# Kernel optimization log

Hardware: AMD Instinct MI355X
Metric: run time of the kernel (lower is better)

## Reference

```python
import jax, jax.numpy as jnp
import numpy as np

B, N, D, DH, H, L = 32768, 6, 128, 64, 4, 4  # batch, items, dim_inp, head/ffn dim, heads, encoders
SEQ = 4  # tokens kept by embeddings[:, :4, :]
EPS = 1e-5


def _layernorm(x, g, b):
    mu = jnp.mean(x, axis=-1, keepdims=True)
    var = jnp.mean((x - mu) ** 2, axis=-1, keepdims=True)
    return (x - mu) / jnp.sqrt(var + EPS) * g + b


def setup_inputs() -> dict:
    key = jax.random.key(0)
    ks = jax.random.split(key, 18)
    s = 0.05
    f32 = jnp.float32
    return {
        "embeddings": jax.random.normal(ks[0], (B, N, D), f32),
        # per-layer, per-head QKV projections: [L, H, D, DH]
        "wq": jax.random.normal(ks[1], (L, H, D, DH), f32) * s,
        "bq": jax.random.normal(ks[2], (L, H, DH), f32) * s,
        "wk": jax.random.normal(ks[3], (L, H, D, DH), f32) * s,
        "bk": jax.random.normal(ks[4], (L, H, DH), f32) * s,
        "wv": jax.random.normal(ks[5], (L, H, D, DH), f32) * s,
        "bv": jax.random.normal(ks[6], (L, H, DH), f32) * s,
        # output projection after head concat: [L, H*DH, D]
        "wo": jax.random.normal(ks[7], (L, H * DH, D), f32) * s,
        "bo": jax.random.normal(ks[8], (L, D), f32) * s,
        "ln1_g": jnp.ones((L, D), f32),
        "ln1_b": jnp.zeros((L, D), f32),
        # FFN: Linear(D, DH) -> GELU -> Linear(DH, D)
        "ff_w1": jax.random.normal(ks[9], (L, D, DH), f32) * s,
        "ff_b1": jax.random.normal(ks[10], (L, DH), f32) * s,
        "ff_w2": jax.random.normal(ks[11], (L, DH, D), f32) * s,
        "ff_b2": jax.random.normal(ks[12], (L, D), f32) * s,
        "ln2_g": jnp.ones((L, D), f32),
        "ln2_b": jnp.zeros((L, D), f32),
    }


def reference(embeddings, wq, bq, wk, bk, wv, bv, wo, bo,
              ln1_g, ln1_b, ff_w1, ff_b1, ff_w2, ff_b2, ln2_g, ln2_b):
    x = embeddings[:, :SEQ, :]          # [B, 4, D]
    positive_pair = embeddings[:, 4, :]  # [B, D]
    negative_pairs = embeddings[:, 5:, :]  # [B, 1, D]

    # Original AttentionHead scales by sqrt(seq_len) (query.size(1)), not sqrt(head_dim)
    scale = jnp.sqrt(jnp.asarray(SEQ, x.dtype))

    for l in range(L):
        # all heads batched into one einsum (same math as per-head Linear+bmm loop)
        q = jnp.einsum('bsd,hdf->bhsf', x, wq[l]) + bq[l][:, None, :]
        k = jnp.einsum('bsd,hdf->bhsf', x, wk[l]) + bk[l][:, None, :]
        v = jnp.einsum('bsd,hdf->bhsf', x, wv[l]) + bv[l][:, None, :]
        scores = jnp.einsum('bhsf,bhtf->bhst', q, k) / scale  # [B,H,4,4]
        attn = jax.nn.softmax(scores, axis=-1)
        ctx = jnp.einsum('bhst,bhtf->bhsf', attn, v)
        # torch.cat over heads along last dim == [B,S,H,DH] -> [B,S,H*DH]
        ctx = ctx.transpose(0, 2, 1, 3).reshape(x.shape[0], SEQ, H * DH)
        proj = ctx @ wo[l] + bo[l]
        context = _layernorm(x + proj, ln1_g[l], ln1_b[l])
        # FFN (dropout = identity in eval); GELU is exact (erf) as in torch default
        h = jax.nn.gelu(context @ ff_w1[l] + ff_b1[l], approximate=False)
        res = h @ ff_w2[l] + ff_b2[l]
        # NOTE: residual uses the PRE-attention input (faithful to Encoder.forward)
        x = _layernorm(res + x, ln2_g[l], ln2_b[l])

    final_embedding = x.mean(axis=-2)  # [B, D]
    return (final_embedding, positive_pair, negative_pairs)
```

## Files before the change

### kernel.cpp

```cpp
#include <hip/hip_runtime.h>
#include <stdint.h>


typedef __attribute__((ext_vector_type(8))) short    bf16x8;
typedef __attribute__((ext_vector_type(4))) _Float16 f16x4;
typedef __attribute__((ext_vector_type(4))) float    f32x4;

#define MFMA_BF(a,b,c) __builtin_amdgcn_mfma_f32_16x16x32_bf16((a),(b),(c),0,0,0)
#define MFMA_H(a,b,c)  __builtin_amdgcn_mfma_f32_16x16x16f16((a),(b),(c),0,0,0)

__device__ __forceinline__ unsigned short f2bf(float f){
  unsigned u = __float_as_uint(f);
  u += 0x7FFFu + ((u>>16)&1u);
  return (unsigned short)(u>>16);
}
__device__ __forceinline__ unsigned pk2bf(float a, float b){
  return (unsigned)f2bf(a) | ((unsigned)f2bf(b)<<16);
}
__device__ __forceinline__ unsigned pkh(float a, float b){
  auto h = __builtin_amdgcn_cvt_pkrtz(a, b);
  return __builtin_bit_cast(unsigned, h);
}
__device__ __forceinline__ void ubf2(unsigned u, float& a, float& b){
  a = __uint_as_float(u<<16);
  b = __uint_as_float(u & 0xffff0000u);
}

__global__ __launch_bounds__(256) void prep_kernel(
    const float* __restrict__ wq, const float* __restrict__ wk,
    const float* __restrict__ wv, const float* __restrict__ wo,
    const float* __restrict__ w1, const float* __restrict__ w2,
    unsigned short* __restrict__ ws){
  int e16 = blockIdx.x*256 + threadIdx.x;
  int t    = e16 >> 10;
  int c    = (e16 >> 6) & 15;
  int lane = e16 & 63;
  int lnid = lane & 15, qid = lane >> 4;
  int l = t/18, r = t - l*18;
  float v[8];
  if (r < 16){
    int h = r >> 2, ty = r & 3;
    if (ty < 3){
      const float* W = (ty==0? wq : (ty==1? wk : wv)) + (size_t)(l*4+h)*8192;
      int f = (c>>2)*16 + lnid, d0 = (c&3)*32 + qid*8;
      #pragma unroll
      for (int j=0;j<8;++j) v[j] = W[(d0+j)*64 + f];
    } else {
      const float* W = wo + (size_t)l*32768 + (size_t)h*8192;
      int dd = (c>>1)*16 + lnid, k0 = (c&1)*32 + qid*8;
      #pragma unroll
      for (int j=0;j<8;++j) v[j] = W[(k0+j)*128 + dd];
    }
  } else if (r == 16){
    const float* W = w1 + (size_t)l*8192;
    int f = (c>>2)*16 + lnid, d0 = (c&3)*32 + qid*8;
    #pragma unroll
    for (int j=0;j<8;++j) v[j] = W[(d0+j)*64 + f];
  } else {
    const float* W = w2 + (size_t)l*8192;
    int dd = (c>>1)*16 + lnid, k0 = (c&1)*32 + qid*8;
    #pragma unroll
    for (int j=0;j<8;++j) v[j] = W[(k0+j)*128 + dd];
  }
  uint4 o;
  o.x = pk2bf(v[0],v[1]); o.y = pk2bf(v[2],v[3]);
  o.z = pk2bf(v[4],v[5]); o.w = pk2bf(v[6],v[7]);
  ((uint4*)ws)[e16] = o;
}

#define XOFF  0
#define QOFF  4352
#define KOFF  6656
#define VOFF  8960
#define PG    11520
#define WSOFF 46080
#define SLOTSZ 16384
#define LDSSZ 78848

__global__ __launch_bounds__(256,2) void bert_kernel(
    const float* __restrict__ emb,
    const float* __restrict__ bq, const float* __restrict__ bk, const float* __restrict__ bv,
    const float* __restrict__ bo,
    const float* __restrict__ ln1g, const float* __restrict__ ln1b,
    const float* __restrict__ fb1, const float* __restrict__ fb2,
    const float* __restrict__ ln2g, const float* __restrict__ ln2b,
    const unsigned short* __restrict__ ws,
    float* __restrict__ out)
{
  __shared__ __align__(16) char smem[LDSSZ];
  const int tid  = threadIdx.x;
  const int wid  = tid>>6;
  const int lane = tid&63;
  const int lnid = lane&15;
  const int qid  = lane>>4;
  const int batch0 = blockIdx.x*16;
  char* gb = smem + wid*PG;
  const f32x4 ZV = {0.f,0.f,0.f,0.f};

  {
    int row = lane>>2, colq = (lane&3)*32;
    const float* src = emb + ((size_t)(batch0 + wid*4 + (row>>2))*6 + (row&3))*128 + colq;
    #pragma unroll
    for (int i=0;i<8;++i){
      float4 v = *(const float4*)(src + i*4);
      uint2 u; u.x = pk2bf(v.x,v.y); u.y = pk2bf(v.z,v.w);
      *(uint2*)(gb + XOFF + row*272 + (colq+i*4)*2) = u;
    }
  }
  {
    const float* eb = emb + (size_t)batch0*768;
    float* o1 = out + 4194304 + (size_t)batch0*128;
    float* o2 = out + 8388608 + (size_t)batch0*128;
    #pragma unroll
    for (int i=0;i<4;++i){
      int idx = i*256 + tid;
      int b = idx>>6, rem = idx&63;
      float4 v = *(const float4*)(eb + b*768 + 512 + rem*4);
      if (rem<32) *(float4*)(o1 + b*128 + rem*4) = v;
      else        *(float4*)(o2 + b*128 + (rem-32)*4) = v;
    }
  }

  const uint4* wsv = (const uint4*)ws;
  {
    #pragma unroll
    for (int i=0;i<4;++i)
      *(uint4*)(smem + WSOFF + (i*256+tid)*16) = wsv[i*256+tid];
  }
  __syncthreads();

  f32x4  pacc[8];
  bf16x8 xfrag[4];
  int sidx = 0;

  for (int l=0; l<4; ++l){
    #pragma unroll
    for (int kc=0;kc<4;++kc)
      xfrag[kc] = *(const bf16x8*)(gb + XOFF + lnid*272 + kc*64 + qid*16);
    #pragma unroll
    for (int nt=0;nt<8;++nt) pacc[nt] = ZV;

    for (int ph=0; ph<18; ++ph){
      char* slot = smem + WSOFF + (sidx&1)*SLOTSZ;

      uint4 pf0,pf1,pf2,pf3;
      bool havepf = (sidx+1 < 72);
      if (havepf){
        const uint4* p = wsv + (size_t)(sidx+1)*1024 + tid;
        pf0 = p[0]; pf1 = p[256]; pf2 = p[512]; pf3 = p[768];
      }

      if (ph < 16){
        int h = ph>>2, t = ph&3;
        if (t < 2){
          char* dst = gb + (t? KOFF : QOFF);
          const float* bias_base = (t? bk : bq) + (l*4+h)*64;
          #pragma unroll
          for (int nt=0; nt<4; ++nt){
            f32x4 a = ZV;
            #pragma unroll
            for (int kc=0; kc<4; ++kc){
              bf16x8 wf = *(const bf16x8*)(slot + (nt*4+kc)*1024 + lane*16);
              a = MFMA_BF(wf, xfrag[kc], a);
            }
            f32x4 bs = *(const f32x4*)(bias_base + nt*16 + qid*4);
            uint2 u; u.x = pk2bf(a[0]+bs[0], a[1]+bs[1]);
                     u.y = pk2bf(a[2]+bs[2], a[3]+bs[3]);
            *(uint2*)(dst + lnid*144 + nt*32 + qid*8) = u;
          }
        } else if (t == 2){
          const float* bias_base = bv + (l*4+h)*64;
          #pragma unroll
          for (int nt=0; nt<4; ++nt){
            f32x4 a = ZV;
            #pragma unroll
            for (int kc=0; kc<4; ++kc){
              bf16x8 wf = *(const bf16x8*)(slot + (nt*4+kc)*1024 + lane*16);
              a = MFMA_BF(xfrag[kc], wf, a);
            }
            float b = bias_base[nt*16 + lnid];
            uint2 u; u.x = pkh(a[0]+b, a[1]+b);
                     u.y = pkh(a[2]+b, a[3]+b);
            *(uint2*)(gb + VOFF + (nt*16+lnid)*40 + qid*8) = u;
          }
        } else {
          bf16x8 kf0 = *(const bf16x8*)(gb+KOFF + lnid*144 + qid*16);
          bf16x8 kf1 = *(const bf16x8*)(gb+KOFF + lnid*144 + 64 + qid*16);
          bf16x8 qf0 = *(const bf16x8*)(gb+QOFF + lnid*144 + qid*16);
          bf16x8 qf1 = *(const bf16x8*)(gb+QOFF + lnid*144 + 64 + qid*16);
          f32x4 st = MFMA_BF(kf0, qf0, ZV);
          st = MFMA_BF(kf1, qf1, st);
          float s0=st[0]*0.5f, s1=st[1]*0.5f, s2=st[2]*0.5f, s3=st[3]*0.5f;
          float mx = fmaxf(fmaxf(s0,s1), fmaxf(s2,s3));
          float p0=__expf(s0-mx), p1=__expf(s1-mx), p2=__expf(s2-mx), p3=__expf(s3-mx);
          float inv = 1.f/(p0+p1+p2+p3);
          bool valid = (lnid>>2) == qid;
          p0 = valid? p0*inv:0.f; p1 = valid? p1*inv:0.f;
          p2 = valid? p2*inv:0.f; p3 = valid? p3*inv:0.f;
          union { unsigned u[2]; f16x4 h4; } pu;
          pu.u[0] = pkh(p0,p1);
          pu.u[1] = pkh(p2,p3);
          f16x4 pf = pu.h4;
          #pragma unroll
          for (int ft=0; ft<4; ++ft){
            f16x4 vf = *(const f16x4*)(gb+VOFF + (ft*16+lnid)*40 + qid*8);
            f32x4 c = MFMA_H(vf, pf, ZV);
            uint2 u; u.x = pk2bf(c[0],c[1]); u.y = pk2bf(c[2],c[3]);
            *(uint2*)(gb+QOFF + lnid*144 + ft*32 + qid*8) = u;
          }
          asm volatile("" ::: "memory");
          bf16x8 c0 = *(const bf16x8*)(gb+QOFF + lnid*144 + qid*16);
          bf16x8 c1 = *(const bf16x8*)(gb+QOFF + lnid*144 + 64 + qid*16);
          #pragma unroll
          for (int nt=0; nt<8; ++nt){
            bf16x8 w0 = *(const bf16x8*)(slot + (nt*2+0)*1024 + lane*16);
            bf16x8 w1f= *(const bf16x8*)(slot + (nt*2+1)*1024 + lane*16);
            f32x4 a = pacc[nt];
            a = MFMA_BF(w0, c0, a);
            a = MFMA_BF(w1f, c1, a);
            pacc[nt] = a;
          }
        }
      } else if (ph == 16){
        float sm=0.f, sq=0.f;
        #pragma unroll
        for (int nt=0;nt<8;++nt){
          f32x4 b4 = *(const f32x4*)(bo + l*128 + nt*16 + qid*4);
          uint2 xr = *(const uint2*)(gb+XOFF + lnid*272 + nt*32 + qid*8);
          float x0,x1,x2,x3; ubf2(xr.x,x0,x1); ubf2(xr.y,x2,x3);
          f32x4 a = pacc[nt];
          a[0]+=b4[0]+x0; a[1]+=b4[1]+x1; a[2]+=b4[2]+x2; a[3]+=b4[3]+x3;
          sm += a[0]+a[1]+a[2]+a[3];
          sq += a[0]*a[0]+a[1]*a[1]+a[2]*a[2]+a[3]*a[3];
          pacc[nt] = a;
        }
        sm += __shfl_xor(sm,16); sq += __shfl_xor(sq,16);
        sm += __shfl_xor(sm,32); sq += __shfl_xor(sq,32);
        float mu = sm*(1.f/128.f);
        float rs = rsqrtf(sq*(1.f/128.f) - mu*mu + 1e-5f);
        #pragma unroll
        for (int nt=0;nt<8;++nt){
          f32x4 g4 = *(const f32x4*)(ln1g + l*128 + nt*16 + qid*4);
          f32x4 be = *(const f32x4*)(ln1b + l*128 + nt*16 + qid*4);
          f32x4 a = pacc[nt];
          float v0 = (a[0]-mu)*rs*g4[0]+be[0];
          float v1 = (a[1]-mu)*rs*g4[1]+be[1];
          float v2 = (a[2]-mu)*rs*g4[2]+be[2];
          float v3 = (a[3]-mu)*rs*g4[3]+be[3];
          uint2 u; u.x = pk2bf(v0,v1); u.y = pk2bf(v2,v3);
          *(uint2*)(gb+QOFF + lnid*272 + nt*32 + qid*8) = u;
        }
        asm volatile("" ::: "memory");
        bf16x8 x2f[4];
        #pragma unroll
        for (int kc=0;kc<4;++kc)
          x2f[kc] = *(const bf16x8*)(gb+QOFF + lnid*272 + kc*64 + qid*16);
        #pragma unroll
        for (int nt=0; nt<4; ++nt){
          f32x4 a = ZV;
          #pragma unroll
          for (int kc=0; kc<4; ++kc){
            bf16x8 wf = *(const bf16x8*)(slot + (nt*4+kc)*1024 + lane*16);
            a = MFMA_BF(wf, x2f[kc], a);
          }
          f32x4 b1 = *(const f32x4*)(fb1 + l*64 + nt*16 + qid*4);
          float g0,g1,g2,g3;
          { float x = a[0]+b1[0]; g0 = 0.5f*x*(1.f+erff(x*0.70710678f)); }
          { float x = a[1]+b1[1]; g1 = 0.5f*x*(1.f+erff(x*0.70710678f)); }
          { float x = a[2]+b1[2]; g2 = 0.5f*x*(1.f+erff(x*0.70710678f)); }
          { float x = a[3]+b1[3]; g3 = 0.5f*x*(1.f+erff(x*0.70710678f)); }
          uint2 u; u.x = pk2bf(g0,g1); u.y = pk2bf(g2,g3);
          *(uint2*)(gb+VOFF + lnid*144 + nt*32 + qid*8) = u;
        }
      } else {
        bf16x8 h0  = *(const bf16x8*)(gb+VOFF + lnid*144 + qid*16);
        bf16x8 h1f = *(const bf16x8*)(gb+VOFF + lnid*144 + 64 + qid*16);
        f32x4 racc[8];
        #pragma unroll
        for (int nt=0; nt<8; ++nt){
          bf16x8 w0 = *(const bf16x8*)(slot + (nt*2+0)*1024 + lane*16);
          bf16x8 w1f= *(const bf16x8*)(slot + (nt*2+1)*1024 + lane*16);
          f32x4 a = MFMA_BF(w0, h0, ZV);
          a = MFMA_BF(w1f, h1f, a);
          racc[nt] = a;
        }
        float sm=0.f, sq=0.f;
        #pragma unroll
        for (int nt=0;nt<8;++nt){
          f32x4 b4 = *(const f32x4*)(fb2 + l*128 + nt*16 + qid*4);
          uint2 xr = *(const uint2*)(gb+XOFF + lnid*272 + nt*32 + qid*8);
          float x0,x1,x2,x3; ubf2(xr.x,x0,x1); ubf2(xr.y,x2,x3);
          f32x4 a = racc[nt];
          a[0]+=b4[0]+x0; a[1]+=b4[1]+x1; a[2]+=b4[2]+x2; a[3]+=b4[3]+x3;
          sm += a[0]+a[1]+a[2]+a[3];
          sq += a[0]*a[0]+a[1]*a[1]+a[2]*a[2]+a[3]*a[3];
          racc[nt] = a;
        }
        sm += __shfl_xor(sm,16); sq += __shfl_xor(sq,16);
        sm += __shfl_xor(sm,32); sq += __shfl_xor(sq,32);
        float mu = sm*(1.f/128.f);
        float rs = rsqrtf(sq*(1.f/128.f) - mu*mu + 1e-5f);
        #pragma unroll
        for (int nt=0;nt<8;++nt){
          f32x4 g4 = *(const f32x4*)(ln2g + l*128 + nt*16 + qid*4);
          f32x4 be = *(const f32x4*)(ln2b + l*128 + nt*16 + qid*4);
          f32x4 a = racc[nt];
          float v0 = (a[0]-mu)*rs*g4[0]+be[0];
          float v1 = (a[1]-mu)*rs*g4[1]+be[1];
          float v2 = (a[2]-mu)*rs*g4[2]+be[2];
          float v3 = (a[3]-mu)*rs*g4[3]+be[3];
          uint2 u; u.x = pk2bf(v0,v1); u.y = pk2bf(v2,v3);
          *(uint2*)(gb+XOFF + lnid*272 + nt*32 + qid*8) = u;
        }
      }

      if (havepf){
        char* ns = smem + WSOFF + ((sidx+1)&1)*SLOTSZ;
        uint4* q = (uint4*)(ns) + tid;
        q[0]=pf0; q[256]=pf1; q[512]=pf2; q[768]=pf3;
      }
      __syncthreads();
      ++sidx;
    }
  }

  {
    int bl = lane>>4;
    float acc[8] = {0,0,0,0,0,0,0,0};
    #pragma unroll
    for (int s=0;s<4;++s){
      uint4 u = *(const uint4*)(gb + XOFF + (bl*4+s)*272 + lnid*16);
      float a0,a1;
      ubf2(u.x,a0,a1); acc[0]+=a0; acc[1]+=a1;
      ubf2(u.y,a0,a1); acc[2]+=a0; acc[3]+=a1;
      ubf2(u.z,a0,a1); acc[4]+=a0; acc[5]+=a1;
      ubf2(u.w,a0,a1); acc[6]+=a0; acc[7]+=a1;
    }
    float* dst = out + (size_t)(batch0 + wid*4 + bl)*128 + lnid*8;
    f32x4 v0 = {acc[0]*0.25f, acc[1]*0.25f, acc[2]*0.25f, acc[3]*0.25f};
    f32x4 v1 = {acc[4]*0.25f, acc[5]*0.25f, acc[6]*0.25f, acc[7]*0.25f};
    *(f32x4*)dst = v0;
    *(f32x4*)(dst+4) = v1;
  }
}

extern "C" void kernel_launch(void* const* d_in, const int* in_sizes, int n_in,
                              void* d_out, int out_size, void* d_ws, size_t ws_size,
                              hipStream_t stream) {
  const float* emb  = (const float*)d_in[0];
  const float* wq   = (const float*)d_in[1];
  const float* bq   = (const float*)d_in[2];
  const float* wk   = (const float*)d_in[3];
  const float* bk   = (const float*)d_in[4];
  const float* wv   = (const float*)d_in[5];
  const float* bv   = (const float*)d_in[6];
  const float* wo   = (const float*)d_in[7];
  const float* bo   = (const float*)d_in[8];
  const float* ln1g = (const float*)d_in[9];
  const float* ln1b = (const float*)d_in[10];
  const float* fw1  = (const float*)d_in[11];
  const float* fb1  = (const float*)d_in[12];
  const float* fw2  = (const float*)d_in[13];
  const float* fb2  = (const float*)d_in[14];
  const float* ln2g = (const float*)d_in[15];
  const float* ln2b = (const float*)d_in[16];
  unsigned short* ws = (unsigned short*)d_ws;
  float* out = (float*)d_out;

  prep_kernel<<<288, 256, 0, stream>>>(wq, wk, wv, wo, fw1, fw2, ws);
  bert_kernel<<<2048, 256, 0, stream>>>(emb, bq, bk, bv, bo, ln1g, ln1b,
                                        fb1, fb2, ln2g, ln2b, ws, out);
}
```

Before: 637.0 us.

## Stream weights from global straight into registers, drop LDS weight staging

Each wave now loads its weight fragments for the next phase directly from global memory into a 16-entry register array, replacing the double-buffered LDS slots and the per-phase block-wide barrier. The phase loop is fully unrolled so the register indexing stays static. LDS use shrinks enough that launch bounds go from 2 to 3 blocks per CU, aiming for higher occupancy and no barrier stalls. In exchange every wave fetches all weights separately, which relies on L1/L2 hits, adds register pressure from holding 16 fragments at once, and exposes global load latency that is no longer covered by the cross-wave prefetch.

```diff
diff --git a/kernel.cpp b/kernel.cpp
--- a/kernel.cpp
+++ b/kernel.cpp
@@ -73,11 +73,9 @@
 #define KOFF  6656
 #define VOFF  8960
 #define PG    11520
-#define WSOFF 46080
-#define SLOTSZ 16384
-#define LDSSZ 78848
-
-__global__ __launch_bounds__(256,2) void bert_kernel(
+#define LDSSZ 46080
+
+__global__ __launch_bounds__(256,3) void bert_kernel(
     const float* __restrict__ emb,
     const float* __restrict__ bq, const float* __restrict__ bk, const float* __restrict__ bv,
     const float* __restrict__ bo,
@@ -121,17 +119,14 @@
     }
   }
 
-  const uint4* wsv = (const uint4*)ws;
-  {
-    #pragma unroll
-    for (int i=0;i<4;++i)
-      *(uint4*)(smem + WSOFF + (i*256+tid)*16) = wsv[i*256+tid];
-  }
-  __syncthreads();
+  const char* wb = (const char*)ws;
+  const int lo16 = lane*16;
+  bf16x8 w[16];
+  #pragma unroll
+  for (int c=0;c<16;++c) w[c] = *(const bf16x8*)(wb + c*1024 + lo16);
 
   f32x4  pacc[8];
   bf16x8 xfrag[4];
-  int sidx = 0;
 
   for (int l=0; l<4; ++l){
     #pragma unroll
@@ -140,16 +135,8 @@
     #pragma unroll
     for (int nt=0;nt<8;++nt) pacc[nt] = ZV;
 
+    #pragma unroll
     for (int ph=0; ph<18; ++ph){
-      char* slot = smem + WSOFF + (sidx&1)*SLOTSZ;
-
-      uint4 pf0,pf1,pf2,pf3;
-      bool havepf = (sidx+1 < 72);
-      if (havepf){
-        const uint4* p = wsv + (size_t)(sidx+1)*1024 + tid;
-        pf0 = p[0]; pf1 = p[256]; pf2 = p[512]; pf3 = p[768];
-      }
-
       if (ph < 16){
         int h = ph>>2, t = ph&3;
         if (t < 2){
@@ -159,10 +146,8 @@
           for (int nt=0; nt<4; ++nt){
             f32x4 a = ZV;
             #pragma unroll
-            for (int kc=0; kc<4; ++kc){
-              bf16x8 wf = *(const bf16x8*)(slot + (nt*4+kc)*1024 + lane*16);
-              a = MFMA_BF(wf, xfrag[kc], a);
-            }
+            for (int kc=0; kc<4; ++kc)
+              a = MFMA_BF(w[nt*4+kc], xfrag[kc], a);
             f32x4 bs = *(const f32x4*)(bias_base + nt*16 + qid*4);
             uint2 u; u.x = pk2bf(a[0]+bs[0], a[1]+bs[1]);
                      u.y = pk2bf(a[2]+bs[2], a[3]+bs[3]);
@@ -174,10 +159,8 @@
           for (int nt=0; nt<4; ++nt){
             f32x4 a = ZV;
             #pragma unroll
-            for (int kc=0; kc<4; ++kc){
-              bf16x8 wf = *(const bf16x8*)(slot + (nt*4+kc)*1024 + lane*16);
-              a = MFMA_BF(xfrag[kc], wf, a);
-            }
+            for (int kc=0; kc<4; ++kc)
+              a = MFMA_BF(xfrag[kc], w[nt*4+kc], a);
             float b = bias_base[nt*16 + lnid];
             uint2 u; u.x = pkh(a[0]+b, a[1]+b);
                      u.y = pkh(a[2]+b, a[3]+b);
@@ -213,11 +196,9 @@
           bf16x8 c1 = *(const bf16x8*)(gb+QOFF + lnid*144 + 64 + qid*16);
           #pragma unroll
           for (int nt=0; nt<8; ++nt){
-            bf16x8 w0 = *(const bf16x8*)(slot + (nt*2+0)*1024 + lane*16);
-            bf16x8 w1f= *(const bf16x8*)(slot + (nt*2+1)*1024 + lane*16);
             f32x4 a = pacc[nt];
-            a = MFMA_BF(w0, c0, a);
-            a = MFMA_BF(w1f, c1, a);
+            a = MFMA_BF(w[nt*2+0], c0, a);
+            a = MFMA_BF(w[nt*2+1], c1, a);
             pacc[nt] = a;
           }
         }
@@ -259,10 +240,8 @@
         for (int nt=0; nt<4; ++nt){
           f32x4 a = ZV;
           #pragma unroll
-          for (int kc=0; kc<4; ++kc){
-            bf16x8 wf = *(const bf16x8*)(slot + (nt*4+kc)*1024 + lane*16);
-            a = MFMA_BF(wf, x2f[kc], a);
-          }
+          for (int kc=0; kc<4; ++kc)
+            a = MFMA_BF(w[nt*4+kc], x2f[kc], a);
           f32x4 b1 = *(const f32x4*)(fb1 + l*64 + nt*16 + qid*4);
           float g0,g1,g2,g3;
           { float x = a[0]+b1[0]; g0 = 0.5f*x*(1.f+erff(x*0.70710678f)); }
@@ -272,16 +251,15 @@
           uint2 u; u.x = pk2bf(g0,g1); u.y = pk2bf(g2,g3);
           *(uint2*)(gb+VOFF + lnid*144 + nt*32 + qid*8) = u;
         }
+        asm volatile("" ::: "memory");
       } else {
         bf16x8 h0  = *(const bf16x8*)(gb+VOFF + lnid*144 + qid*16);
         bf16x8 h1f = *(const bf16x8*)(gb+VOFF + lnid*144 + 64 + qid*16);
         f32x4 racc[8];
         #pragma unroll
         for (int nt=0; nt<8; ++nt){
-          bf16x8 w0 = *(const bf16x8*)(slot + (nt*2+0)*1024 + lane*16);
-          bf16x8 w1f= *(const bf16x8*)(slot + (nt*2+1)*1024 + lane*16);
-          f32x4 a = MFMA_BF(w0, h0, ZV);
-          a = MFMA_BF(w1f, h1f, a);
+          f32x4 a = MFMA_BF(w[nt*2+0], h0, ZV);
+          a = MFMA_BF(w[nt*2+1], h1f, a);
           racc[nt] = a;
         }
         float sm=0.f, sq=0.f;
@@ -312,15 +290,14 @@
           uint2 u; u.x = pk2bf(v0,v1); u.y = pk2bf(v2,v3);
           *(uint2*)(gb+XOFF + lnid*272 + nt*32 + qid*8) = u;
         }
+        asm volatile("" ::: "memory");
       }
 
-      if (havepf){
-        char* ns = smem + WSOFF + ((sidx+1)&1)*SLOTSZ;
-        uint4* q = (uint4*)(ns) + tid;
-        q[0]=pf0; q[256]=pf1; q[512]=pf2; q[768]=pf3;
+      wb += 16384;
+      if (l < 3 || ph < 17){
+        #pragma unroll
+        for (int c=0;c<16;++c) w[c] = *(const bf16x8*)(wb + c*1024 + lo16);
       }
-      __syncthreads();
-      ++sidx;
     }
   }
 
```

Measured after the change: 714.0 us. 12.1% more time.
